# Performance work log

Hardware: AMD Instinct MI355X
Metric: run time of the kernel (lower is better)

Reference implementation:

```python
import jax, jax.numpy as jnp
import numpy as np

B, T, D, NH = 4, 2048, 768, 12
DH = D // NH
NEG = -100000.0  # module uses masked_fill with -100000.0, not -inf


def setup_inputs() -> dict:
    key = jax.random.key(0)
    ks = jax.random.split(key, 9)
    s = 1.0 / np.sqrt(D)
    return {
        "x": jax.random.normal(ks[0], (B, T, D), jnp.float32),
        "wq": jax.random.normal(ks[1], (D, D), jnp.float32) * s,
        "bq": jax.random.normal(ks[2], (D,), jnp.float32) * 0.02,
        "wk": jax.random.normal(ks[3], (D, D), jnp.float32) * s,
        "bk": jax.random.normal(ks[4], (D,), jnp.float32) * 0.02,
        "wv": jax.random.normal(ks[5], (D, D), jnp.float32) * s,
        "bv": jax.random.normal(ks[6], (D,), jnp.float32) * 0.02,
        "wo": jax.random.normal(ks[7], (D, D), jnp.float32) * s,
        "bo": jax.random.normal(ks[8], (D,), jnp.float32) * 0.02,
    }


def reference(x, wq, bq, wk, bk, wv, bv, wo, bo):
    Bx, Tx, E = x.shape
    # torch Linear: y = x @ W.T + b, weight shape [out, in]
    def heads(w, b):
        return (x @ w.T + b).reshape(Bx, Tx, NH, DH).transpose(0, 2, 1, 3)  # [B,nh,T,dh]
    Q, K, V = heads(wq, bq), heads(wk, bk), heads(wv, bv)
    scale = 1.0 / jnp.sqrt(jnp.float32(DH))
    QK = jnp.einsum("bhqd,bhkd->bhqk", Q, K) * scale  # [B,nh,T,T]
    causal = jnp.tril(jnp.ones((Tx, Tx), dtype=bool))
    QK = jnp.where(causal, QK, NEG)
    A = jax.nn.softmax(QK, axis=-1)  # attn_dropout p=0 (eval)
    Z = jnp.einsum("bhqk,bhkd->bhqd", A, V)
    Z = Z.transpose(0, 2, 1, 3).reshape(Bx, Tx, E)
    return Z @ wo.T + bo  # resid_dropout p=0 (eval)
```

## Files before the change

kernel.cpp:

```cpp
#include <hip/hip_runtime.h>


#define B_ 4
#define T_ 2048
#define D_ 768
#define NH_ 12
#define DH_ 64
#define M_ (B_ * T_)

typedef __attribute__((ext_vector_type(8))) short bf16x8;
typedef __attribute__((ext_vector_type(4))) float f32x4;
typedef __attribute__((ext_vector_type(16))) float f32x16;
typedef __attribute__((ext_vector_type(4))) unsigned int u32x4;

__device__ __forceinline__ unsigned short f2bf(float f) {
  unsigned int u = __builtin_bit_cast(unsigned int, f);
  u += 0x7FFFu + ((u >> 16) & 1u);
  return (unsigned short)(u >> 16);
}

__device__ __forceinline__ void async16(const void* g, void* l) {
  __builtin_amdgcn_global_load_lds(
      (const __attribute__((address_space(1))) unsigned int*)g,
      (__attribute__((address_space(3))) unsigned int*)l, 16, 0, 0);
}

__global__ void cvt_kernel(const float* __restrict__ x, const float* __restrict__ wq,
                           const float* __restrict__ wk, const float* __restrict__ wv,
                           const float* __restrict__ wo,
                           unsigned short* __restrict__ xb, unsigned short* __restrict__ wqb,
                           unsigned short* __restrict__ wkb, unsigned short* __restrict__ wvb,
                           unsigned short* __restrict__ wob) {
  const float* src; unsigned short* dst; int n4;
  switch (blockIdx.y) {
    case 0: src = x;  dst = xb;  n4 = M_ * D_ / 4; break;
    case 1: src = wq; dst = wqb; n4 = D_ * D_ / 4; break;
    case 2: src = wk; dst = wkb; n4 = D_ * D_ / 4; break;
    case 3: src = wv; dst = wvb; n4 = D_ * D_ / 4; break;
    default: src = wo; dst = wob; n4 = D_ * D_ / 4; break;
  }
  int stride = gridDim.x * blockDim.x;
  for (int i = blockIdx.x * blockDim.x + threadIdx.x; i < n4; i += stride) {
    float4 v = ((const float4*)src)[i];
    ushort4 o;
    o.x = f2bf(v.x); o.y = f2bf(v.y); o.z = f2bf(v.z); o.w = f2bf(v.w);
    ((ushort4*)dst)[i] = o;
  }
}

__global__ __launch_bounds__(256) void gemm_kernel(
    const unsigned short* __restrict__ A,
    const unsigned short* __restrict__ W0, const unsigned short* __restrict__ W1,
    const unsigned short* __restrict__ W2,
    const float* __restrict__ bias0, const float* __restrict__ bias1,
    const float* __restrict__ bias2,
    void* out0, void* out1, void* out2,
    float s0, float s1, float s2,
    int M, int N, int K, int qkv) {
  __shared__ __align__(16) unsigned short As[2][128 * 64];
  __shared__ __align__(16) unsigned short Bs[2][128 * 64];

  int bid = blockIdx.x;
  int xcd = bid & 7, g = bid >> 3;
  int mt, nt, y;
  if (qkv) { mt = xcd + ((g / 18) << 3); int sub = g % 18; y = sub / 6; nt = sub % 6; }
  else     { mt = xcd + ((g / 6) << 3);  nt = g % 6; y = 0; }

  const unsigned short* W = y == 0 ? W0 : (y == 1 ? W1 : W2);
  const float* bias = y == 0 ? bias0 : (y == 1 ? bias1 : bias2);
  void* outp = y == 0 ? out0 : (y == 1 ? out1 : out2);
  float scl = y == 0 ? s0 : (y == 1 ? s1 : s2);
  int mode = qkv ? ((y == 2) ? 2 : 1) : 0;

  int tid = threadIdx.x, lane = tid & 63, w = tid >> 6;
  int l15 = lane & 15, l4 = lane >> 4;
  int wr = w >> 1, wc = w & 1;

  int m0 = mt << 7;
  int n0 = nt << 7;

  f32x4 acc[4][4] = {};

  int sRow[4], sCol[4];
#pragma unroll
  for (int c = 0; c < 4; ++c) {
    int pos = ((c * 4 + w) * 64 + lane) * 8;
    int row = pos >> 6, colE = pos & 63;
    sRow[c] = row;
    sCol[c] = colE ^ ((row & 7) << 3);
  }

#pragma unroll
  for (int c = 0; c < 4; ++c) {
    async16(A + (size_t)(m0 + sRow[c]) * K + sCol[c], (char*)As[0] + (c * 4 + w) * 1024);
    async16(W + (size_t)(n0 + sRow[c]) * K + sCol[c], (char*)Bs[0] + (c * 4 + w) * 1024);
  }

  int nkt = K >> 6;
#pragma unroll 1
  for (int t = 0; t < nkt; ++t) {
    int cur = t & 1;
    __syncthreads();
    if (t + 1 < nkt) {
      int kt1 = (t + 1) << 6;
#pragma unroll
      for (int c = 0; c < 4; ++c) {
        async16(A + (size_t)(m0 + sRow[c]) * K + kt1 + sCol[c],
                (char*)As[cur ^ 1] + (c * 4 + w) * 1024);
        async16(W + (size_t)(n0 + sRow[c]) * K + kt1 + sCol[c],
                (char*)Bs[cur ^ 1] + (c * 4 + w) * 1024);
      }
    }
#pragma unroll
    for (int ks = 0; ks < 2; ++ks) {
      bf16x8 af[4], bfr[4];
#pragma unroll
      for (int m = 0; m < 4; ++m) {
        int row = wr * 64 + m * 16 + l15;
        int cb = (ks * 64 + l4 * 16) ^ ((row & 7) << 4);
        af[m] = *(const bf16x8*)((const char*)As[cur] + row * 128 + cb);
      }
#pragma unroll
      for (int n = 0; n < 4; ++n) {
        int row = wc * 64 + n * 16 + l15;
        int cb = (ks * 64 + l4 * 16) ^ ((row & 7) << 4);
        bfr[n] = *(const bf16x8*)((const char*)Bs[cur] + row * 128 + cb);
      }
#pragma unroll
      for (int m = 0; m < 4; ++m)
#pragma unroll
        for (int n = 0; n < 4; ++n)
          acc[m][n] = __builtin_amdgcn_mfma_f32_16x16x32_bf16(af[m], bfr[n], acc[m][n], 0, 0, 0);
    }
  }

  if (mode == 2) {
#pragma unroll
    for (int n = 0; n < 4; ++n) {
      int col = n0 + wc * 64 + n * 16 + l15;
      float bv = bias[col];
      int h = col >> 6, d = col & 63;
#pragma unroll
      for (int m = 0; m < 4; ++m) {
        int rbase = m0 + wr * 64 + m * 16 + l4 * 4;
        int bb = rbase >> 11, t = rbase & (T_ - 1);
        ushort4 o;
        o.x = f2bf(acc[m][n][0] + bv);
        o.y = f2bf(acc[m][n][1] + bv);
        o.z = f2bf(acc[m][n][2] + bv);
        o.w = f2bf(acc[m][n][3] + bv);
        *(ushort4*)((unsigned short*)outp + ((size_t)(bb * NH_ + h) * DH_ + d) * T_ + t) = o;
      }
    }
  } else {
#pragma unroll
    for (int n = 0; n < 4; ++n) {
      int col = n0 + wc * 64 + n * 16 + l15;
      float bv = bias[col];
#pragma unroll
      for (int m = 0; m < 4; ++m) {
        int rbase = m0 + wr * 64 + m * 16 + l4 * 4;
#pragma unroll
        for (int r = 0; r < 4; ++r) {
          float v = (acc[m][n][r] + bv) * scl;
          size_t idx = (size_t)(rbase + r) * N + col;
          if (mode == 1) ((unsigned short*)outp)[idx] = f2bf(v);
          else           ((float*)outp)[idx] = v;
        }
      }
    }
  }
}

__global__ __launch_bounds__(256, 2) void attn_kernel(
    const unsigned short* __restrict__ Q, const unsigned short* __restrict__ Kg,
    const unsigned short* __restrict__ VT, unsigned short* __restrict__ Z) {
  __shared__ __align__(16) char lds[57344];

  int tid = threadIdx.x, lane = tid & 63, w = tid >> 6;
  int l31 = lane & 31, hi = lane >> 5;
  int bid = blockIdx.x;
  int xcd = bid & 7, g = bid >> 3;
  int qt = 15 - g / 6;
  int bh = xcd + (g % 6) * 8;
  int b = bh / NH_, h = bh % NH_;
  int q0 = qt * 128;
  int qrow = q0 + w * 32 + l31;

  const unsigned short* Qb = Q + (size_t)(b * T_) * D_ + h * DH_;
  const unsigned short* Kb = Kg + (size_t)(b * T_) * D_ + h * DH_;
  const unsigned short* VTb = VT + (size_t)(b * NH_ + h) * DH_ * T_;

  bf16x8 qf[4];
#pragma unroll
  for (int s = 0; s < 4; ++s)
    qf[s] = *(const bf16x8*)(Qb + (size_t)qrow * D_ + s * 16 + hi * 8);

  int sRow[2], sCol[2];
#pragma unroll
  for (int c = 0; c < 2; ++c) {
    int pos = ((c * 4 + w) * 64 + lane) * 8;
    int row = pos >> 6, colE = pos & 63;
    sRow[c] = row;
    sCol[c] = colE ^ ((row & 7) << 3);
  }

  int koff[2][4];
#pragma unroll
  for (int n = 0; n < 2; ++n)
#pragma unroll
    for (int s = 0; s < 4; ++s) {
      int row = n * 32 + l31;
      koff[n][s] = row * 128 + ((s * 32 + hi * 16) ^ ((row & 7) << 4));
    }

  f32x16 zt[2] = {};
  float l_run = 0.f;
  int ntiles = 2 * qt + 2;

#pragma unroll
  for (int c = 0; c < 2; ++c) {
    async16(Kb + (size_t)sRow[c] * D_ + sCol[c], lds + 0 + (c * 4 + w) * 1024);
    async16(VTb + (size_t)sRow[c] * T_ + sCol[c], lds + 16384 + (c * 4 + w) * 1024);
  }

#define ATTN_TILE(KCUR, VCUR, KNXT, VNXT)                                              \
  do {                                                                                 \
    __syncthreads();          \
    if (t + 1 < ntiles) {                                                              \
      int kv1 = (t + 1) * 64;                                                          \
      _Pragma("unroll") for (int c = 0; c < 2; ++c) {                                  \
        async16(Kb + (size_t)(kv1 + sRow[c]) * D_ + sCol[c],                           \
                lds + KNXT + (c * 4 + w) * 1024);                                      \
        async16(VTb + (size_t)sRow[c] * T_ + kv1 + sCol[c],                            \
                lds + VNXT + (c * 4 + w) * 1024);                                      \
      }                                                                                \
    }                                                                                  \
    f32x16 st[2];                                                                      \
    __builtin_amdgcn_s_setprio(1);                                                     \
    _Pragma("unroll") for (int n = 0; n < 2; ++n) {                                    \
      f32x16 a = {};                                                                   \
      _Pragma("unroll") for (int s = 0; s < 4; ++s) {                                  \
        bf16x8 kf = *(const bf16x8*)(lds + KCUR + koff[n][s]);                         \
        a = __builtin_amdgcn_mfma_f32_32x32x16_bf16(kf, qf[s], a, 0, 0, 0);            \
      }                                                                                \
      st[n] = a;                                                                       \
    }                                                                                  \
    __builtin_amdgcn_s_setprio(0);                                                     \
    if (t >= 2 * qt) {                            \
      int kvb = t * 64;                                                                \
      _Pragma("unroll") for (int n = 0; n < 2; ++n)                                    \
        _Pragma("unroll") for (int m = 0; m < 4; ++m)                                  \
          _Pragma("unroll") for (int c2 = 0; c2 < 4; ++c2) {                           \
            int kv = kvb + n * 32 + m * 8 + hi * 4 + c2;                               \
            if (kv > qrow) st[n][m * 4 + c2] = -1e30f;                                 \
          }                                                                            \
    }                                                                                  \
    bf16x8 pb[4];                                                                      \
    _Pragma("unroll") for (int n = 0; n < 2; ++n) {                                    \
      float u[16];                                                                     \
      _Pragma("unroll") for (int r = 0; r < 16; ++r) {                                 \
        u[r] = __builtin_amdgcn_exp2f(st[n][r]);                                       \
        l_run += u[r];                                                                 \
      }                                                                                \
      _Pragma("unroll") for (int hf = 0; hf < 2; ++hf) {                               \
        unsigned int A0, A1, B0, B1;                                                   \
        asm("v_cvt_pk_bf16_f32 %0, %1, %2" : "=v"(A0) : "v"(u[hf*8+0]), "v"(u[hf*8+1]));\
        asm("v_cvt_pk_bf16_f32 %0, %1, %2" : "=v"(A1) : "v"(u[hf*8+2]), "v"(u[hf*8+3]));\
        asm("v_cvt_pk_bf16_f32 %0, %1, %2" : "=v"(B0) : "v"(u[hf*8+4]), "v"(u[hf*8+5]));\
        asm("v_cvt_pk_bf16_f32 %0, %1, %2" : "=v"(B1) : "v"(u[hf*8+6]), "v"(u[hf*8+7]));\
        asm("v_permlane32_swap_b32 %0, %1" : "+v"(A0), "+v"(B0));                      \
        asm("v_permlane32_swap_b32 %0, %1" : "+v"(A1), "+v"(B1));                      \
        u32x4 pk; pk[0] = A0; pk[1] = A1; pk[2] = B0; pk[3] = B1;                      \
        pb[n * 2 + hf] = __builtin_bit_cast(bf16x8, pk);                               \
      }                                                                                \
    }                                                                                  \
    __builtin_amdgcn_s_setprio(1);                                                     \
    _Pragma("unroll") for (int dt = 0; dt < 2; ++dt) {                                 \
      _Pragma("unroll") for (int s = 0; s < 4; ++s) {                                  \
        bf16x8 vf = *(const bf16x8*)(lds + VCUR + koff[dt][s]);                        \
        zt[dt] = __builtin_amdgcn_mfma_f32_32x32x16_bf16(vf, pb[s], zt[dt], 0, 0, 0);  \
      }                                                                                \
    }                                                                                  \
    __builtin_amdgcn_s_setprio(0);                                                     \
  } while (0)

#pragma unroll 1
  for (int t = 0; t < ntiles; ++t) {
    if ((t & 1) == 0) {
      ATTN_TILE(0, 16384, 8192, 24576);
    } else {
      ATTN_TILE(8192, 24576, 0, 16384);
    }
  }
#undef ATTN_TILE

  l_run += __shfl_xor(l_run, 32);
  float inv = __builtin_amdgcn_rcpf(l_run);
  unsigned short* Zrow = Z + (size_t)(b * T_ + qrow) * D_ + h * DH_;
#pragma unroll
  for (int dt = 0; dt < 2; ++dt)
#pragma unroll
    for (int m = 0; m < 4; ++m) {
      ushort4 o;
      o.x = f2bf(zt[dt][m * 4 + 0] * inv);
      o.y = f2bf(zt[dt][m * 4 + 1] * inv);
      o.z = f2bf(zt[dt][m * 4 + 2] * inv);
      o.w = f2bf(zt[dt][m * 4 + 3] * inv);
      *(ushort4*)(Zrow + dt * 32 + m * 8 + hi * 4) = o;
    }
}

extern "C" void kernel_launch(void* const* d_in, const int* in_sizes, int n_in,
                              void* d_out, int out_size, void* d_ws, size_t ws_size,
                              hipStream_t stream) {
  (void)in_sizes; (void)n_in; (void)out_size; (void)ws_size;
  const float* x  = (const float*)d_in[0];
  const float* wq = (const float*)d_in[1];
  const float* bq = (const float*)d_in[2];
  const float* wk = (const float*)d_in[3];
  const float* bk = (const float*)d_in[4];
  const float* wv = (const float*)d_in[5];
  const float* bv = (const float*)d_in[6];
  const float* wo = (const float*)d_in[7];
  const float* bo = (const float*)d_in[8];

  char* ws = (char*)d_ws;
  const size_t XB = (size_t)M_ * D_ * 2;
  const size_t WB = (size_t)D_ * D_ * 2;
  unsigned short* xb  = (unsigned short*)(ws);
  unsigned short* wqb = (unsigned short*)(ws + XB);
  unsigned short* wkb = (unsigned short*)(ws + XB + WB);
  unsigned short* wvb = (unsigned short*)(ws + XB + 2 * WB);
  unsigned short* wob = (unsigned short*)(ws + XB + 3 * WB);
  unsigned short* Qb  = (unsigned short*)(ws + XB + 4 * WB);
  unsigned short* Kb  = (unsigned short*)(ws + XB + 4 * WB + XB);
  unsigned short* VTb = (unsigned short*)(ws + XB + 4 * WB + 2 * XB);
  unsigned short* Zb  = xb;

  const float SCALE_Q = 0.125f * 1.44269504f;

  cvt_kernel<<<dim3(1024, 5), 256, 0, stream>>>(x, wq, wk, wv, wo, xb, wqb, wkb, wvb, wob);
  gemm_kernel<<<dim3(8 * 8 * 18), 256, 0, stream>>>(
      xb, wqb, wkb, wvb, bq, bk, bv, Qb, Kb, VTb, SCALE_Q, 1.0f, 1.0f, M_, D_, D_, 1);
  attn_kernel<<<dim3(768), 256, 0, stream>>>(Qb, Kb, VTb, Zb);
  gemm_kernel<<<dim3(8 * 8 * 6), 256, 0, stream>>>(
      Zb, wob, wob, wob, bo, bo, bo, d_out, d_out, d_out, 1.0f, 1.0f, 1.0f, M_, D_, D_, 0);
}
```

Before: 121.8 us.

## Switch projection GEMMs to 256x256 tiles with 512 threads and explicit waits

Replaces the 128x128-tile, 256-thread GEMM with a 256x256-tile, 512-thread kernel in which each wave computes a 128x64 sub-tile. The intent is to raise data reuse per LDS load and per global byte. The loop now uses raw barriers with explicit vmcnt waits, so the next tile's async loads overlap the current tile's math, and it raises wave priority around the MFMA block. The cost is a much smaller grid: 288 blocks for QKV and 96 for the output projection. That risks leaving many CUs idle, and the 128KB LDS footprint limits occupancy.

Measured after the change: 146.2 us. 20.0% more time.

```diff
diff --git a/kernel.cpp b/kernel.cpp
--- a/kernel.cpp
+++ b/kernel.cpp
@@ -24,6 +24,13 @@
       (const __attribute__((address_space(1))) unsigned int*)g,
       (__attribute__((address_space(3))) unsigned int*)l, 16, 0, 0);
 }
+
+#define RAW_BARRIER()                         \
+  do {                                        \
+    asm volatile("" ::: "memory");            \
+    __builtin_amdgcn_s_barrier();             \
+    asm volatile("" ::: "memory");            \
+  } while (0)
 
 __global__ void cvt_kernel(const float* __restrict__ x, const float* __restrict__ wq,
                            const float* __restrict__ wk, const float* __restrict__ wv,
@@ -48,122 +55,137 @@
   }
 }
 
-__global__ __launch_bounds__(256) void gemm_kernel(
+__global__ __launch_bounds__(512, 2) void gemm256_kernel(
     const unsigned short* __restrict__ A,
     const unsigned short* __restrict__ W0, const unsigned short* __restrict__ W1,
     const unsigned short* __restrict__ W2,
     const float* __restrict__ bias0, const float* __restrict__ bias1,
     const float* __restrict__ bias2,
     void* out0, void* out1, void* out2,
-    float s0, float s1, float s2,
-    int M, int N, int K, int qkv) {
-  __shared__ __align__(16) unsigned short As[2][128 * 64];
-  __shared__ __align__(16) unsigned short Bs[2][128 * 64];
+    float s0, int K, int qkv) {
+  __shared__ __align__(16) unsigned short As[2][256 * 64];
+  __shared__ __align__(16) unsigned short Bs[2][256 * 64];
 
   int bid = blockIdx.x;
   int xcd = bid & 7, g = bid >> 3;
-  int mt, nt, y;
-  if (qkv) { mt = xcd + ((g / 18) << 3); int sub = g % 18; y = sub / 6; nt = sub % 6; }
-  else     { mt = xcd + ((g / 6) << 3);  nt = g % 6; y = 0; }
-
+  int mt, nt;
+  if (qkv) { mt = xcd + (g / 9) * 8; nt = g % 9; }
+  else     { mt = xcd + (g / 3) * 8; nt = g % 3; }
+  int y  = qkv ? nt / 3 : 0;
+  int nW = qkv ? nt % 3 : nt;
   const unsigned short* W = y == 0 ? W0 : (y == 1 ? W1 : W2);
   const float* bias = y == 0 ? bias0 : (y == 1 ? bias1 : bias2);
   void* outp = y == 0 ? out0 : (y == 1 ? out1 : out2);
-  float scl = y == 0 ? s0 : (y == 1 ? s1 : s2);
+  float scl = (qkv && y == 0) ? s0 : 1.0f;
   int mode = qkv ? ((y == 2) ? 2 : 1) : 0;
 
-  int tid = threadIdx.x, lane = tid & 63, w = tid >> 6;
+  int tid = threadIdx.x, lane = tid & 63, wid = tid >> 6;
   int l15 = lane & 15, l4 = lane >> 4;
-  int wr = w >> 1, wc = w & 1;
-
-  int m0 = mt << 7;
-  int n0 = nt << 7;
-
-  f32x4 acc[4][4] = {};
+  int wm = wid >> 2, wn = wid & 3;
+  int m0 = mt << 8, n0w = nW << 8;
 
   int sRow[4], sCol[4];
 #pragma unroll
   for (int c = 0; c < 4; ++c) {
-    int pos = ((c * 4 + w) * 64 + lane) * 8;
-    int row = pos >> 6, colE = pos & 63;
+    int u = c * 8 + wid;
+    int row = u * 8 + (lane >> 3);
+    int colE = (lane & 7) * 8;
     sRow[c] = row;
     sCol[c] = colE ^ ((row & 7) << 3);
   }
 
-#pragma unroll
-  for (int c = 0; c < 4; ++c) {
-    async16(A + (size_t)(m0 + sRow[c]) * K + sCol[c], (char*)As[0] + (c * 4 + w) * 1024);
-    async16(W + (size_t)(n0 + sRow[c]) * K + sCol[c], (char*)Bs[0] + (c * 4 + w) * 1024);
-  }
-
-  int nkt = K >> 6;
+  int aoff[8], boff[4];
+#pragma unroll
+  for (int mf = 0; mf < 8; ++mf) {
+    int row = wm * 128 + mf * 16 + l15;
+    aoff[mf] = row * 128 + ((l4 * 16) ^ ((row & 7) << 4));
+  }
+#pragma unroll
+  for (int nf = 0; nf < 4; ++nf) {
+    int row = wn * 64 + nf * 16 + l15;
+    boff[nf] = row * 128 + ((l4 * 16) ^ ((row & 7) << 4));
+  }
+
+  f32x4 acc[8][4] = {};
+
+#pragma unroll
+  for (int c = 0; c < 4; ++c)
+    async16(A + (size_t)(m0 + sRow[c]) * K + sCol[c], (char*)As[0] + (c * 8 + wid) * 1024);
+#pragma unroll
+  for (int c = 0; c < 4; ++c)
+    async16(W + (size_t)(n0w + sRow[c]) * K + sCol[c], (char*)Bs[0] + (c * 8 + wid) * 1024);
+
+  int NT = K >> 6;
 #pragma unroll 1
-  for (int t = 0; t < nkt; ++t) {
+  for (int t = 0; t < NT; ++t) {
     int cur = t & 1;
-    __syncthreads();
-    if (t + 1 < nkt) {
+    RAW_BARRIER();
+    if (t + 1 < NT) {
       int kt1 = (t + 1) << 6;
 #pragma unroll
-      for (int c = 0; c < 4; ++c) {
+      for (int c = 0; c < 4; ++c)
         async16(A + (size_t)(m0 + sRow[c]) * K + kt1 + sCol[c],
-                (char*)As[cur ^ 1] + (c * 4 + w) * 1024);
-        async16(W + (size_t)(n0 + sRow[c]) * K + kt1 + sCol[c],
-                (char*)Bs[cur ^ 1] + (c * 4 + w) * 1024);
+                (char*)As[cur ^ 1] + (c * 8 + wid) * 1024);
+#pragma unroll
+      for (int c = 0; c < 4; ++c)
+        async16(W + (size_t)(n0w + sRow[c]) * K + kt1 + sCol[c],
+                (char*)Bs[cur ^ 1] + (c * 8 + wid) * 1024);
+      asm volatile("s_waitcnt vmcnt(8)" ::: "memory");
+    } else {
+      asm volatile("s_waitcnt vmcnt(0)" ::: "memory");
+    }
+    RAW_BARRIER();
+    const char* Ab = (const char*)As[cur];
+    const char* Bb = (const char*)Bs[cur];
+#pragma unroll
+    for (int ks = 0; ks < 2; ++ks) {
+      bf16x8 af[8], bf[4];
+#pragma unroll
+      for (int mf = 0; mf < 8; ++mf)
+        af[mf] = *(const bf16x8*)(Ab + (aoff[mf] ^ (ks << 6)));
+#pragma unroll
+      for (int nf = 0; nf < 4; ++nf)
+        bf[nf] = *(const bf16x8*)(Bb + (boff[nf] ^ (ks << 6)));
+      __builtin_amdgcn_s_setprio(1);
+#pragma unroll
+      for (int mf = 0; mf < 8; ++mf)
+#pragma unroll
+        for (int nf = 0; nf < 4; ++nf)
+          acc[mf][nf] = __builtin_amdgcn_mfma_f32_16x16x32_bf16(af[mf], bf[nf], acc[mf][nf], 0, 0, 0);
+      __builtin_amdgcn_s_setprio(0);
+    }
+  }
+
+  if (mode == 2) {
+#pragma unroll
+    for (int nf = 0; nf < 4; ++nf) {
+      int colW = n0w + wn * 64 + nf * 16 + l15;
+      float bv = bias[colW];
+      int h = colW >> 6, d = colW & 63;
+#pragma unroll
+      for (int mf = 0; mf < 8; ++mf) {
+        int rbase = m0 + wm * 128 + mf * 16 + l4 * 4;
+        int bb = rbase >> 11, tt = rbase & (T_ - 1);
+        ushort4 o;
+        o.x = f2bf(acc[mf][nf][0] + bv);
+        o.y = f2bf(acc[mf][nf][1] + bv);
+        o.z = f2bf(acc[mf][nf][2] + bv);
+        o.w = f2bf(acc[mf][nf][3] + bv);
+        *(ushort4*)((unsigned short*)outp + ((size_t)(bb * NH_ + h) * DH_ + d) * T_ + tt) = o;
       }
     }
-#pragma unroll
-    for (int ks = 0; ks < 2; ++ks) {
-      bf16x8 af[4], bfr[4];
-#pragma unroll
-      for (int m = 0; m < 4; ++m) {
-        int row = wr * 64 + m * 16 + l15;
-        int cb = (ks * 64 + l4 * 16) ^ ((row & 7) << 4);
-        af[m] = *(const bf16x8*)((const char*)As[cur] + row * 128 + cb);
-      }
-#pragma unroll
-      for (int n = 0; n < 4; ++n) {
-        int row = wc * 64 + n * 16 + l15;
-        int cb = (ks * 64 + l4 * 16) ^ ((row & 7) << 4);
-        bfr[n] = *(const bf16x8*)((const char*)Bs[cur] + row * 128 + cb);
-      }
-#pragma unroll
-      for (int m = 0; m < 4; ++m)
-#pragma unroll
-        for (int n = 0; n < 4; ++n)
-          acc[m][n] = __builtin_amdgcn_mfma_f32_16x16x32_bf16(af[m], bfr[n], acc[m][n], 0, 0, 0);
-    }
-  }
-
-  if (mode == 2) {
-#pragma unroll
-    for (int n = 0; n < 4; ++n) {
-      int col = n0 + wc * 64 + n * 16 + l15;
-      float bv = bias[col];
-      int h = col >> 6, d = col & 63;
-#pragma unroll
-      for (int m = 0; m < 4; ++m) {
-        int rbase = m0 + wr * 64 + m * 16 + l4 * 4;
-        int bb = rbase >> 11, t = rbase & (T_ - 1);
-        ushort4 o;
-        o.x = f2bf(acc[m][n][0] + bv);
-        o.y = f2bf(acc[m][n][1] + bv);
-        o.z = f2bf(acc[m][n][2] + bv);
-        o.w = f2bf(acc[m][n][3] + bv);
-        *(ushort4*)((unsigned short*)outp + ((size_t)(bb * NH_ + h) * DH_ + d) * T_ + t) = o;
-      }
-    }
   } else {
 #pragma unroll
-    for (int n = 0; n < 4; ++n) {
-      int col = n0 + wc * 64 + n * 16 + l15;
-      float bv = bias[col];
-#pragma unroll
-      for (int m = 0; m < 4; ++m) {
-        int rbase = m0 + wr * 64 + m * 16 + l4 * 4;
+    for (int nf = 0; nf < 4; ++nf) {
+      int colW = n0w + wn * 64 + nf * 16 + l15;
+      float bv = bias[colW];
+#pragma unroll
+      for (int mf = 0; mf < 8; ++mf) {
+        int rbase = m0 + wm * 128 + mf * 16 + l4 * 4;
 #pragma unroll
         for (int r = 0; r < 4; ++r) {
-          float v = (acc[m][n][r] + bv) * scl;
-          size_t idx = (size_t)(rbase + r) * N + col;
+          float v = (acc[mf][nf][r] + bv) * scl;
+          size_t idx = (size_t)(rbase + r) * D_ + colW;
           if (mode == 1) ((unsigned short*)outp)[idx] = f2bf(v);
           else           ((float*)outp)[idx] = v;
         }
@@ -341,9 +363,9 @@
   const float SCALE_Q = 0.125f * 1.44269504f;
 
   cvt_kernel<<<dim3(1024, 5), 256, 0, stream>>>(x, wq, wk, wv, wo, xb, wqb, wkb, wvb, wob);
-  gemm_kernel<<<dim3(8 * 8 * 18), 256, 0, stream>>>(
-      xb, wqb, wkb, wvb, bq, bk, bv, Qb, Kb, VTb, SCALE_Q, 1.0f, 1.0f, M_, D_, D_, 1);
+  gemm256_kernel<<<dim3(288), 512, 0, stream>>>(
+      xb, wqb, wkb, wvb, bq, bk, bv, Qb, Kb, VTb, SCALE_Q, D_, 1);
   attn_kernel<<<dim3(768), 256, 0, stream>>>(Qb, Kb, VTb, Zb);
-  gemm_kernel<<<dim3(8 * 8 * 6), 256, 0, stream>>>(
-      Zb, wob, wob, wob, bo, bo, bo, d_out, d_out, d_out, 1.0f, 1.0f, 1.0f, M_, D_, D_, 0);
-}
+  gemm256_kernel<<<dim3(96), 512, 0, stream>>>(
+      Zb, wob, wob, wob, bo, bo, bo, d_out, d_out, d_out, 1.0f, D_, 0);
+}
```
